# Performance work log

Measured on AMD Instinct MI355X. Metric: run time of the kernel, lower is better.

Reference implementation:

```python
import jax, jax.numpy as jnp
import numpy as np

D_IN = 4096
D_OUT = 4096
RANK = 16
NUM_EXPERTS = 8
TOP_K = 2
SCALING = 32.0 / RANK  # lora_alpha / r = 2.0


def setup_inputs() -> dict:
    key = jax.random.key(0)
    ks = jax.random.split(key, 6)
    x = jax.random.normal(ks[0], (4, 2048, D_IN), dtype=jnp.float32)
    W_base = jax.random.normal(ks[1], (D_OUT, D_IN), dtype=jnp.float32) * (1.0 / np.sqrt(D_IN))
    b_base = jax.random.normal(ks[2], (D_OUT,), dtype=jnp.float32) * 0.01
    W_router = jax.random.normal(ks[3], (NUM_EXPERTS, D_IN), dtype=jnp.float32) * 0.01
    # kaiming-uniform-like A; B nonzero (module inits B to zero, but zero B makes outputs/grads trivial)
    A_stack = jax.random.uniform(ks[4], (NUM_EXPERTS, RANK, D_IN), dtype=jnp.float32,
                                 minval=-1.0, maxval=1.0) * (1.0 / np.sqrt(D_IN))
    B_stack = jax.random.normal(ks[5], (NUM_EXPERTS, D_OUT, RANK), dtype=jnp.float32) * 0.02
    return {"x": x, "W_base": W_base, "b_base": b_base,
            "W_router": W_router, "A_stack": A_stack, "B_stack": B_stack}


def reference(x, W_base, b_base, W_router, A_stack, B_stack):
    orig_shape = x.shape
    xf = x.reshape(-1, D_IN)                                # [N, d_in]
    # Router: softmax -> top-k -> renormalize
    logits = xf @ W_router.T                                # [N, E]
    probs = jax.nn.softmax(logits, axis=-1)
    topk_p, topk_i = jax.lax.top_k(probs, TOP_K)            # [N, K]
    topk_p = topk_p / jnp.sum(topk_p, axis=-1, keepdims=True)
    # Combine weights per expert (scatter top-k probs into [N, E])
    combine = jnp.sum(jax.nn.one_hot(topk_i, NUM_EXPERTS, dtype=xf.dtype)
                      * topk_p[..., None], axis=1)          # [N, E]
    # Low-rank expert path: x @ A_e^T, weight, then @ B_e^T, summed over experts
    h = jnp.einsum('nd,erd->ner', xf, A_stack)              # [N, E, r]
    h = h * combine[..., None]
    lora_out = jnp.einsum('ner,eor->no', h, B_stack) * SCALING  # [N, d_out]
    base_out = xf @ W_base.T + b_base                       # [N, d_out]
    out = base_out + lora_out
    return out.reshape(orig_shape[:-1] + (D_OUT,))
```

## Files before the change

### kernel.cpp

```cpp
#include <hip/hip_runtime.h>

#define D_IN   4096
#define D_OUT  4096
#define N_TOK  8192
#define RANK   16
#define NEXP   8
#define ER     128
#define KCAT   4224
#define SCALING 2.0f

typedef __attribute__((ext_vector_type(8))) short short8;
typedef __attribute__((ext_vector_type(4))) float f32x4;
typedef __attribute__((ext_vector_type(4))) unsigned short us4;
typedef unsigned int uint;

__device__ __forceinline__ unsigned short f2bf(float f) {
  unsigned u = __float_as_uint(f);
  u += 0x7FFFu + ((u >> 16) & 1u);
  return (unsigned short)(u >> 16);
}

__device__ __forceinline__ void gload_lds16(const void* g, void* l) {
  __builtin_amdgcn_global_load_lds(
      (const __attribute__((address_space(1))) unsigned int*)g,
      (__attribute__((address_space(3))) unsigned int*)l, 16, 0, 0);
}

__global__ __launch_bounds__(256) void fused_prep_router_kernel(
    const float* __restrict__ X, const float* __restrict__ Wr,
    const float* __restrict__ W, const float* __restrict__ A,
    const float* __restrict__ B,
    unsigned short* __restrict__ Xcat, float* __restrict__ Comb,
    unsigned short* __restrict__ Wcat, unsigned short* __restrict__ Ab) {
  if (blockIdx.x < 512) {
    int wave = threadIdx.x >> 6, lane = threadIdx.x & 63;
    int tok0 = blockIdx.x * 16 + wave * 4;
    float acc[4][8];
#pragma unroll
    for (int t = 0; t < 4; ++t)
#pragma unroll
      for (int e = 0; e < 8; ++e) acc[t][e] = 0.f;
    const float4* X4 = (const float4*)X;
    const float4* W4 = (const float4*)Wr;
#pragma unroll 1
    for (int it = 0; it < 16; ++it) {
      int kq = it * 64 + lane;
      float4 w[8];
#pragma unroll
      for (int e = 0; e < 8; ++e) w[e] = W4[e * 1024 + kq];
#pragma unroll
      for (int t = 0; t < 4; ++t) {
        float4 xv = X4[(size_t)(tok0 + t) * 1024 + kq];
        us4 xb = { f2bf(xv.x), f2bf(xv.y), f2bf(xv.z), f2bf(xv.w) };
        ((us4*)(Xcat + (size_t)(tok0 + t) * KCAT))[kq] = xb;
#pragma unroll
        for (int e = 0; e < 8; ++e)
          acc[t][e] = fmaf(xv.x, w[e].x, fmaf(xv.y, w[e].y,
                       fmaf(xv.z, w[e].z, fmaf(xv.w, w[e].w, acc[t][e]))));
      }
    }
#pragma unroll
    for (int t = 0; t < 4; ++t)
#pragma unroll
      for (int e = 0; e < 8; ++e) {
        float v = acc[t][e];
        for (int off = 32; off; off >>= 1) v += __shfl_xor(v, off, 64);
        acc[t][e] = v;
      }
#pragma unroll
    for (int t = 0; t < 4; ++t) {
      float m1 = acc[t][0]; int i1 = 0;
#pragma unroll
      for (int e = 1; e < 8; ++e) if (acc[t][e] > m1) { m1 = acc[t][e]; i1 = e; }
      float m2 = -1e30f; int i2 = 0;
#pragma unroll
      for (int e = 0; e < 8; ++e)
        if (e != i1 && acc[t][e] > m2) { m2 = acc[t][e]; i2 = e; }
      float w1 = 1.f / (1.f + expf(m2 - m1));
      if (lane < 8) {
        float v = (lane == i1) ? w1 : (lane == i2) ? (1.f - w1) : 0.f;
        Comb[(size_t)(tok0 + t) * 8 + lane] = v * SCALING;
      }
    }
  } else {
    const int NW4 = (D_OUT * D_IN) / 4;
    const int NA4 = (ER * D_IN) / 4;
    const int NB4 = (D_OUT * ER) / 4;
    const int total = NW4 + NA4 + NB4;
    const int stride = 2048 * 256;
    for (int i = (blockIdx.x - 512) * blockDim.x + threadIdx.x; i < total;
         i += stride) {
      if (i < NW4) {
        float4 v = ((const float4*)W)[i];
        us4 o = { f2bf(v.x), f2bf(v.y), f2bf(v.z), f2bf(v.w) };
        int row = i >> 10, kq = i & 1023;
        ((us4*)(Wcat + (size_t)row * KCAT))[kq] = o;
      } else if (i < NW4 + NA4) {
        int j = i - NW4;
        float4 v = ((const float4*)A)[j];
        us4 o = { f2bf(v.x), f2bf(v.y), f2bf(v.z), f2bf(v.w) };
        ((us4*)Ab)[j] = o;
      } else {
        int j = i - NW4 - NA4;
        int o = j >> 5; int rem = j & 31; int e = rem >> 2; int rq = rem & 3;
        float4 v = *(const float4*)(B + (size_t)e * D_OUT * RANK + o * RANK + rq * 4);
        us4 ob = { f2bf(v.x), f2bf(v.y), f2bf(v.z), f2bf(v.w) };
        *(us4*)(Wcat + (size_t)o * KCAT + D_IN + e * 16 + rq * 4) = ob;
      }
    }
  }
}

#define HSTG(S) { const uint hbase = (S) * 40960u; \
  _Pragma("unroll") for (int c = 0; c < 2; ++c) { gload_lds16(pa[c], ldsc + hbase + da[c]); pa[c] += 128; } \
  _Pragma("unroll") for (int c = 0; c < 8; ++c) { gload_lds16(pb[c], ldsc + hbase + db[c]); pb[c] += 128; } }

#define HTILE(S, S2, DOSTG, VM) { const uint hb = (S) * 40960u; \
  short8 af[4]; short8 bfr[4][4]; \
  _Pragma("unroll") for (int kk = 0; kk < 4; ++kk) af[kk] = *(const short8*)(ldsc + hb + oA[kk]); \
  _Pragma("unroll") for (int n = 0; n < 4; ++n) \
    _Pragma("unroll") for (int kk = 0; kk < 4; ++kk) bfr[n][kk] = *(const short8*)(ldsc + hb + oB[n][kk]); \
  if (DOSTG) HSTG(S2); \
  __builtin_amdgcn_sched_barrier(0); __builtin_amdgcn_s_barrier(); __builtin_amdgcn_sched_barrier(0); \
  __builtin_amdgcn_s_setprio(1); \
  _Pragma("unroll") for (int kk = 0; kk < 4; ++kk) \
    _Pragma("unroll") for (int n = 0; n < 4; ++n) \
      acc[n] = __builtin_amdgcn_mfma_f32_16x16x32_bf16(af[kk], bfr[n][kk], acc[n], 0, 0, 0); \
  __builtin_amdgcn_s_setprio(0); \
  __builtin_amdgcn_sched_barrier(0); \
  asm volatile("s_waitcnt vmcnt(" #VM ")" ::: ); \
  __builtin_amdgcn_s_barrier(); __builtin_amdgcn_sched_barrier(0); }

__global__ __launch_bounds__(256, 1) void h_gemm_kernel(
    unsigned short* Xcat, const unsigned short* __restrict__ Ab,
    const float* __restrict__ Comb) {
  __shared__ unsigned short hlds[61440];
  char* ldsc = (char*)hlds;
  const int tid = threadIdx.x, wave = tid >> 6, lane = tid & 63;
  const int wm = wave >> 1, wn = wave & 1;
  const int row0 = blockIdx.x * 32;

  const unsigned short* pa[2]; uint da[2];
#pragma unroll
  for (int c = 0; c < 2; ++c) {
    int ch = c * 256 + tid, row = ch >> 4, s = ch & 15;
    pa[c] = Xcat + (size_t)(row0 + row) * KCAT + (s ^ ((row >> 1) & 7)) * 8;
    da[c] = (uint)ch * 16;
  }
  const unsigned short* pb[8]; uint db[8];
#pragma unroll
  for (int c = 0; c < 8; ++c) {
    int ch = c * 256 + tid, row = ch >> 4, s = ch & 15;
    pb[c] = Ab + (size_t)row * D_IN + (s ^ ((row >> 1) & 7)) * 8;
    db[c] = 8192u + (uint)ch * 16;
  }

  uint oA[4], oB[4][4];
  {
    int rA = wm * 16 + (lane & 15);
#pragma unroll
    for (int kk = 0; kk < 4; ++kk) {
      int slot = kk * 4 + (lane >> 4);
      oA[kk] = (uint)rA * 256 + (uint)((slot ^ ((rA >> 1) & 7)) * 16);
    }
#pragma unroll
    for (int n = 0; n < 4; ++n) {
      int rB = wn * 64 + n * 16 + (lane & 15);
#pragma unroll
      for (int kk = 0; kk < 4; ++kk) {
        int slot = kk * 4 + (lane >> 4);
        oB[n][kk] = 8192u + (uint)rB * 256 + (uint)((slot ^ ((rB >> 1) & 7)) * 16);
      }
    }
  }

  f32x4 acc[4];
#pragma unroll
  for (int n = 0; n < 4; ++n) acc[n] = (f32x4){0.f, 0.f, 0.f, 0.f};

  HSTG(0); HSTG(1);
  asm volatile("s_waitcnt vmcnt(10)" ::: );
  __builtin_amdgcn_s_barrier();
  __builtin_amdgcn_sched_barrier(0);

#pragma unroll 1
  for (int i3 = 0; i3 < 10; ++i3) {
    HTILE(0, 2, 1, 10);
    HTILE(1, 0, 1, 10);
    HTILE(2, 1, 1, 10);
  }
  HTILE(0, 0, 0, 0);
  HTILE(1, 0, 0, 0);

#pragma unroll
  for (int n = 0; n < 4; ++n) {
    int c = wn * 64 + n * 16 + (lane & 15);
    int e = c >> 4;
#pragma unroll
    for (int i = 0; i < 4; ++i) {
      int r = row0 + wm * 16 + (lane >> 4) * 4 + i;
      float v = acc[n][i] * Comb[(size_t)r * 8 + e];
      Xcat[(size_t)r * KCAT + D_IN + c] = f2bf(v);
    }
  }
}

#define STG_A(S) { gload_lds16(pA0, ldsc + (S) * 32768u + dA0); pA0 += 32; \
                   gload_lds16(pA1, ldsc + (S) * 32768u + dA1); pA1 += 32; }
#define STG_B(S) { gload_lds16(pB0, ldsc + (S) * 32768u + dB0); pB0 += 32; \
                   gload_lds16(pB1, ldsc + (S) * 32768u + dB1); pB1 += 32; }

#define MTILE(SLOT, SLOT3, DOSTG, VM) { \
  const uint sb = (SLOT) * 32768u; \
  short8 a0[4], bf[4], a1[4]; \
  _Pragma("unroll") for (int m = 0; m < 4; ++m) a0[m] = *(const short8*)(ldsc + sb + offA[m]); \
  _Pragma("unroll") for (int n = 0; n < 4; ++n) bf[n] = *(const short8*)(ldsc + sb + offB[n]); \
  _Pragma("unroll") for (int m = 0; m < 4; ++m) a1[m] = *(const short8*)(ldsc + sb + offA[4 + m]); \
  if (DOSTG) STG_A(SLOT3); \
  __builtin_amdgcn_sched_barrier(0); \
  __builtin_amdgcn_s_barrier(); \
  __builtin_amdgcn_sched_barrier(0); \
  __builtin_amdgcn_s_setprio(1); \
  _Pragma("unroll") for (int m = 0; m < 4; ++m) \
    _Pragma("unroll") for (int n = 0; n < 4; ++n) \
      acc[m][n] = __builtin_amdgcn_mfma_f32_16x16x32_bf16(a0[m], bf[n], acc[m][n], 0, 0, 0); \
  __builtin_amdgcn_s_setprio(0); \
  __builtin_amdgcn_sched_barrier(0); \
  __builtin_amdgcn_s_barrier(); \
  __builtin_amdgcn_sched_barrier(0); \
  if (DOSTG) STG_B(SLOT3); \
  __builtin_amdgcn_sched_barrier(0); \
  __builtin_amdgcn_s_barrier(); \
  __builtin_amdgcn_sched_barrier(0); \
  __builtin_amdgcn_s_setprio(1); \
  _Pragma("unroll") for (int m = 0; m < 4; ++m) \
    _Pragma("unroll") for (int n = 0; n < 4; ++n) \
      acc[4 + m][n] = __builtin_amdgcn_mfma_f32_16x16x32_bf16(a1[m], bf[n], acc[4 + m][n], 0, 0, 0); \
  __builtin_amdgcn_s_setprio(0); \
  __builtin_amdgcn_sched_barrier(0); \
  asm volatile("s_waitcnt vmcnt(" #VM ")" ::: ); \
  __builtin_amdgcn_s_barrier(); \
  __builtin_amdgcn_sched_barrier(0); }

__global__ __launch_bounds__(512, 2) void main_gemm_kernel(
    const unsigned short* __restrict__ Xcat, const unsigned short* __restrict__ Wcat,
    const float* __restrict__ bias, float* __restrict__ Out) {
  __shared__ unsigned short lds[4 * 16384];
  char* ldsc = (char*)lds;
  const int tid = threadIdx.x;
  const int wave = tid >> 6, lane = tid & 63;
  const int wm = wave >> 2, wn = wave & 3;
  const int ks = lane >> 4;

  int bid = blockIdx.x;
  int swz = (bid & 7) * 64 + (bid >> 3);
  int mb = swz >> 4, nb = swz & 15;
  const int row0 = mb * 256, col0 = nb * 256;

  const unsigned short *pA0, *pA1, *pB0, *pB1;
  uint dA0, dA1, dB0, dB1;
  {
    int ch0 = tid, ch1 = 512 + tid;
    int rr0 = ch0 >> 2, ss0 = (ch0 & 3) ^ ((ch0 >> 3) & 3);
    int rr1 = ch1 >> 2, ss1 = (ch1 & 3) ^ ((ch1 >> 3) & 3);
    pA0 = Xcat + (size_t)(row0 + rr0) * KCAT + ss0 * 8;
    pA1 = Xcat + (size_t)(row0 + rr1) * KCAT + ss1 * 8;
    pB0 = Wcat + (size_t)(col0 + rr0) * KCAT + ss0 * 8;
    pB1 = Wcat + (size_t)(col0 + rr1) * KCAT + ss1 * 8;
    dA0 = (uint)wave * 1024;          dA1 = 8192u + (uint)wave * 1024;
    dB0 = 16384u + (uint)wave * 1024; dB1 = 24576u + (uint)wave * 1024;
  }

  uint offA[8], offB[4];
#pragma unroll
  for (int mi = 0; mi < 8; ++mi) {
    int r = wm * 128 + mi * 16 + (lane & 15);
    offA[mi] = (uint)r * 64 + (uint)((ks ^ ((r >> 1) & 3)) * 16);
  }
#pragma unroll
  for (int ni = 0; ni < 4; ++ni) {
    int r = wn * 64 + ni * 16 + (lane & 15);
    offB[ni] = 16384u + (uint)r * 64 + (uint)((ks ^ ((r >> 1) & 3)) * 16);
  }

  f32x4 acc[8][4];
#pragma unroll
  for (int mi = 0; mi < 8; ++mi)
#pragma unroll
    for (int ni = 0; ni < 4; ++ni) acc[mi][ni] = (f32x4){0.f, 0.f, 0.f, 0.f};

  STG_A(0); STG_B(0); STG_A(1); STG_B(1); STG_A(2); STG_B(2);
  asm volatile("s_waitcnt vmcnt(8)" ::: );
  __builtin_amdgcn_s_barrier();
  __builtin_amdgcn_sched_barrier(0);

#pragma unroll 1
  for (int i4 = 0; i4 < 32; ++i4) {
    MTILE(0, 3, 1, 8);
    MTILE(1, 0, 1, 8);
    MTILE(2, 1, 1, 8);
    MTILE(3, 2, 1, 8);
  }
  MTILE(0, 3, 1, 8);
  MTILE(1, 0, 0, 4);
  MTILE(2, 0, 0, 0);
  MTILE(3, 0, 0, 0);

#pragma unroll
  for (int ni = 0; ni < 4; ++ni) {
    const int c = col0 + wn * 64 + ni * 16 + (lane & 15);
    const float bv = bias[c];
#pragma unroll
    for (int mi = 0; mi < 8; ++mi) {
#pragma unroll
      for (int i = 0; i < 4; ++i) {
        int r = row0 + wm * 128 + mi * 16 + ks * 4 + i;
        Out[(size_t)r * D_OUT + c] = acc[mi][ni][i] + bv;
      }
    }
  }
}

extern "C" void kernel_launch(void* const* d_in, const int* in_sizes, int n_in,
                              void* d_out, int out_size, void* d_ws, size_t ws_size,
                              hipStream_t stream) {
  const float* x        = (const float*)d_in[0];
  const float* W_base   = (const float*)d_in[1];
  const float* b_base   = (const float*)d_in[2];
  const float* W_router = (const float*)d_in[3];
  const float* A_stack  = (const float*)d_in[4];
  const float* B_stack  = (const float*)d_in[5];
  float* out = (float*)d_out;

  char* ws = (char*)d_ws;
  unsigned short* Xcat = (unsigned short*)(ws);
  unsigned short* Wcat = (unsigned short*)(ws + 69206016);
  unsigned short* Ab   = (unsigned short*)(ws + 103809024);
  float*          Comb = (float*)(ws + 104857600);

  hipLaunchKernelGGL(fused_prep_router_kernel, dim3(2560), dim3(256), 0, stream,
                     x, W_router, W_base, A_stack, B_stack, Xcat, Comb, Wcat, Ab);
  hipLaunchKernelGGL(h_gemm_kernel, dim3(256), dim3(256), 0, stream,
                     Xcat, Ab, Comb);
  hipLaunchKernelGGL(main_gemm_kernel, dim3(512), dim3(512), 0, stream,
                     Xcat, Wcat, b_base, out);
}
```

Before: 341.3 us.

## Prefetch next k-tile LDS fragments into ping-pong registers during MFMA phases

Result: no change. 340.4 us (-0.3%).

```diff
diff --git a/kernel.cpp b/kernel.cpp
--- a/kernel.cpp
+++ b/kernel.cpp
@@ -210,35 +210,46 @@
 #define STG_B(S) { gload_lds16(pB0, ldsc + (S) * 32768u + dB0); pB0 += 32; \
                    gload_lds16(pB1, ldsc + (S) * 32768u + dB1); pB1 += 32; }
 
-#define MTILE(SLOT, SLOT3, DOSTG, VM) { \
+#define MT(SLOT, SLOT3, DOSTG, VMTOK, aCur, bCur, aNxt, bNxt, RDNEXT, LGTOK) { \
   const uint sb = (SLOT) * 32768u; \
-  short8 a0[4], bf[4], a1[4]; \
-  _Pragma("unroll") for (int m = 0; m < 4; ++m) a0[m] = *(const short8*)(ldsc + sb + offA[m]); \
-  _Pragma("unroll") for (int n = 0; n < 4; ++n) bf[n] = *(const short8*)(ldsc + sb + offB[n]); \
-  _Pragma("unroll") for (int m = 0; m < 4; ++m) a1[m] = *(const short8*)(ldsc + sb + offA[4 + m]); \
+  const uint sbn = (((SLOT) + 1) & 3) * 32768u; \
+   \
+  _Pragma("unroll") for (int m = 0; m < 4; ++m) \
+    a1r[m] = *(const short8*)(ldsc + sb + offA[4 + m]); \
   if (DOSTG) STG_A(SLOT3); \
   __builtin_amdgcn_sched_barrier(0); \
   __builtin_amdgcn_s_barrier(); \
+  __builtin_amdgcn_sched_barrier(0); \
+  asm volatile("s_waitcnt lgkmcnt(4)" ::: ); \
   __builtin_amdgcn_sched_barrier(0); \
   __builtin_amdgcn_s_setprio(1); \
   _Pragma("unroll") for (int m = 0; m < 4; ++m) \
     _Pragma("unroll") for (int n = 0; n < 4; ++n) \
-      acc[m][n] = __builtin_amdgcn_mfma_f32_16x16x32_bf16(a0[m], bf[n], acc[m][n], 0, 0, 0); \
+      acc[m][n] = __builtin_amdgcn_mfma_f32_16x16x32_bf16(aCur[m], bCur[n], acc[m][n], 0, 0, 0); \
   __builtin_amdgcn_s_setprio(0); \
   __builtin_amdgcn_sched_barrier(0); \
+  asm volatile("s_waitcnt " VMTOK ::: ); \
   __builtin_amdgcn_s_barrier(); \
   __builtin_amdgcn_sched_barrier(0); \
+   \
+  if (RDNEXT) { \
+    _Pragma("unroll") for (int m = 0; m < 4; ++m) \
+      aNxt[m] = *(const short8*)(ldsc + sbn + offA[m]); \
+    _Pragma("unroll") for (int n = 0; n < 4; ++n) \
+      bNxt[n] = *(const short8*)(ldsc + sbn + offB[n]); \
+  } \
   if (DOSTG) STG_B(SLOT3); \
   __builtin_amdgcn_sched_barrier(0); \
   __builtin_amdgcn_s_barrier(); \
+  __builtin_amdgcn_sched_barrier(0); \
+  asm volatile("s_waitcnt " LGTOK ::: ); \
   __builtin_amdgcn_sched_barrier(0); \
   __builtin_amdgcn_s_setprio(1); \
   _Pragma("unroll") for (int m = 0; m < 4; ++m) \
     _Pragma("unroll") for (int n = 0; n < 4; ++n) \
-      acc[4 + m][n] = __builtin_amdgcn_mfma_f32_16x16x32_bf16(a1[m], bf[n], acc[4 + m][n], 0, 0, 0); \
+      acc[4 + m][n] = __builtin_amdgcn_mfma_f32_16x16x32_bf16(a1r[m], bCur[n], acc[4 + m][n], 0, 0, 0); \
   __builtin_amdgcn_s_setprio(0); \
   __builtin_amdgcn_sched_barrier(0); \
-  asm volatile("s_waitcnt vmcnt(" #VM ")" ::: ); \
   __builtin_amdgcn_s_barrier(); \
   __builtin_amdgcn_sched_barrier(0); }
 
@@ -289,22 +300,29 @@
 #pragma unroll
     for (int ni = 0; ni < 4; ++ni) acc[mi][ni] = (f32x4){0.f, 0.f, 0.f, 0.f};
 
+  short8 aAr[4], bAr[4], aBr[4], bBr[4], a1r[4];
+
   STG_A(0); STG_B(0); STG_A(1); STG_B(1); STG_A(2); STG_B(2);
   asm volatile("s_waitcnt vmcnt(8)" ::: );
   __builtin_amdgcn_s_barrier();
   __builtin_amdgcn_sched_barrier(0);
+#pragma unroll
+  for (int m = 0; m < 4; ++m) aAr[m] = *(const short8*)(ldsc + offA[m]);
+#pragma unroll
+  for (int n = 0; n < 4; ++n) bAr[n] = *(const short8*)(ldsc + offB[n]);
+  __builtin_amdgcn_sched_barrier(0);
 
 #pragma unroll 1
   for (int i4 = 0; i4 < 32; ++i4) {
-    MTILE(0, 3, 1, 8);
-    MTILE(1, 0, 1, 8);
-    MTILE(2, 1, 1, 8);
-    MTILE(3, 2, 1, 8);
-  }
-  MTILE(0, 3, 1, 8);
-  MTILE(1, 0, 0, 4);
-  MTILE(2, 0, 0, 0);
-  MTILE(3, 0, 0, 0);
+    MT(0, 3, 1, "vmcnt(6)", aAr, bAr, aBr, bBr, 1, "lgkmcnt(8)");
+    MT(1, 0, 1, "vmcnt(6)", aBr, bBr, aAr, bAr, 1, "lgkmcnt(8)");
+    MT(2, 1, 1, "vmcnt(6)", aAr, bAr, aBr, bBr, 1, "lgkmcnt(8)");
+    MT(3, 2, 1, "vmcnt(6)", aBr, bBr, aAr, bAr, 1, "lgkmcnt(8)");
+  }
+  MT(0, 3, 1, "vmcnt(6)", aAr, bAr, aBr, bBr, 1, "lgkmcnt(8)");
+  MT(1, 0, 0, "vmcnt(4)", aBr, bBr, aAr, bAr, 1, "lgkmcnt(8)");
+  MT(2, 0, 0, "vmcnt(0)", aAr, bAr, aBr, bBr, 1, "lgkmcnt(8)");
+  MT(3, 0, 0, "vmcnt(0)", aBr, bBr, aAr, bAr, 0, "lgkmcnt(0)");
 
 #pragma unroll
   for (int ni = 0; ni < 4; ++ni) {
```

## Shrink main GEMM tile to 128x128 with 4 waves and 3-stage pipeline

Applied to the files above, without the earlier changes.

Measured after the change: 468.9 us. 1.37x slower.

```diff
diff --git a/kernel.cpp b/kernel.cpp
--- a/kernel.cpp
+++ b/kernel.cpp
@@ -205,116 +205,102 @@
   }
 }
 
-#define STG_A(S) { gload_lds16(pA0, ldsc + (S) * 32768u + dA0); pA0 += 32; \
-                   gload_lds16(pA1, ldsc + (S) * 32768u + dA1); pA1 += 32; }
-#define STG_B(S) { gload_lds16(pB0, ldsc + (S) * 32768u + dB0); pB0 += 32; \
-                   gload_lds16(pB1, ldsc + (S) * 32768u + dB1); pB1 += 32; }
-
-#define MTILE(SLOT, SLOT3, DOSTG, VM) { \
-  const uint sb = (SLOT) * 32768u; \
-  short8 a0[4], bf[4], a1[4]; \
-  _Pragma("unroll") for (int m = 0; m < 4; ++m) a0[m] = *(const short8*)(ldsc + sb + offA[m]); \
-  _Pragma("unroll") for (int n = 0; n < 4; ++n) bf[n] = *(const short8*)(ldsc + sb + offB[n]); \
-  _Pragma("unroll") for (int m = 0; m < 4; ++m) a1[m] = *(const short8*)(ldsc + sb + offA[4 + m]); \
-  if (DOSTG) STG_A(SLOT3); \
+#define STG(S) { \
+  gload_lds16(pA0, ldsc + (S) * 16384u + dA0); pA0 += 32; \
+  gload_lds16(pA1, ldsc + (S) * 16384u + dA1); pA1 += 32; \
+  gload_lds16(pB0, ldsc + (S) * 16384u + dB0); pB0 += 32; \
+  gload_lds16(pB1, ldsc + (S) * 16384u + dB1); pB1 += 32; }
+
+#define MT(SLOT, SLOTN, DOSTG, VM) { \
+  const uint sb = (SLOT) * 16384u; \
+  short8 a[4], b[4]; \
+  _Pragma("unroll") for (int m = 0; m < 4; ++m) a[m] = *(const short8*)(ldsc + sb + offA[m]); \
+  _Pragma("unroll") for (int n = 0; n < 4; ++n) b[n] = *(const short8*)(ldsc + sb + offB[n]); \
+  if (DOSTG) STG(SLOTN); \
   __builtin_amdgcn_sched_barrier(0); \
   __builtin_amdgcn_s_barrier(); \
   __builtin_amdgcn_sched_barrier(0); \
   __builtin_amdgcn_s_setprio(1); \
   _Pragma("unroll") for (int m = 0; m < 4; ++m) \
     _Pragma("unroll") for (int n = 0; n < 4; ++n) \
-      acc[m][n] = __builtin_amdgcn_mfma_f32_16x16x32_bf16(a0[m], bf[n], acc[m][n], 0, 0, 0); \
-  __builtin_amdgcn_s_setprio(0); \
-  __builtin_amdgcn_sched_barrier(0); \
-  __builtin_amdgcn_s_barrier(); \
-  __builtin_amdgcn_sched_barrier(0); \
-  if (DOSTG) STG_B(SLOT3); \
-  __builtin_amdgcn_sched_barrier(0); \
-  __builtin_amdgcn_s_barrier(); \
-  __builtin_amdgcn_sched_barrier(0); \
-  __builtin_amdgcn_s_setprio(1); \
-  _Pragma("unroll") for (int m = 0; m < 4; ++m) \
-    _Pragma("unroll") for (int n = 0; n < 4; ++n) \
-      acc[4 + m][n] = __builtin_amdgcn_mfma_f32_16x16x32_bf16(a1[m], bf[n], acc[4 + m][n], 0, 0, 0); \
+      acc[m][n] = __builtin_amdgcn_mfma_f32_16x16x32_bf16(a[m], b[n], acc[m][n], 0, 0, 0); \
   __builtin_amdgcn_s_setprio(0); \
   __builtin_amdgcn_sched_barrier(0); \
   asm volatile("s_waitcnt vmcnt(" #VM ")" ::: ); \
   __builtin_amdgcn_s_barrier(); \
   __builtin_amdgcn_sched_barrier(0); }
 
-__global__ __launch_bounds__(512, 2) void main_gemm_kernel(
+__global__ __launch_bounds__(256, 3) void main_gemm_kernel(
     const unsigned short* __restrict__ Xcat, const unsigned short* __restrict__ Wcat,
     const float* __restrict__ bias, float* __restrict__ Out) {
-  __shared__ unsigned short lds[4 * 16384];
+  __shared__ unsigned short lds[3 * 8192];
   char* ldsc = (char*)lds;
   const int tid = threadIdx.x;
   const int wave = tid >> 6, lane = tid & 63;
-  const int wm = wave >> 2, wn = wave & 3;
+  const int wm = wave >> 1, wn = wave & 1;
   const int ks = lane >> 4;
 
   int bid = blockIdx.x;
-  int swz = (bid & 7) * 64 + (bid >> 3);
-  int mb = swz >> 4, nb = swz & 15;
-  const int row0 = mb * 256, col0 = nb * 256;
+  int swz = (bid & 7) * 256 + (bid >> 3);
+  int mb = swz >> 5, nb = swz & 31;
+  const int row0 = mb * 128, col0 = nb * 128;
 
   const unsigned short *pA0, *pA1, *pB0, *pB1;
   uint dA0, dA1, dB0, dB1;
   {
-    int ch0 = tid, ch1 = 512 + tid;
+    int ch0 = tid, ch1 = 256 + tid;
     int rr0 = ch0 >> 2, ss0 = (ch0 & 3) ^ ((ch0 >> 3) & 3);
     int rr1 = ch1 >> 2, ss1 = (ch1 & 3) ^ ((ch1 >> 3) & 3);
     pA0 = Xcat + (size_t)(row0 + rr0) * KCAT + ss0 * 8;
     pA1 = Xcat + (size_t)(row0 + rr1) * KCAT + ss1 * 8;
     pB0 = Wcat + (size_t)(col0 + rr0) * KCAT + ss0 * 8;
     pB1 = Wcat + (size_t)(col0 + rr1) * KCAT + ss1 * 8;
-    dA0 = (uint)wave * 1024;          dA1 = 8192u + (uint)wave * 1024;
-    dB0 = 16384u + (uint)wave * 1024; dB1 = 24576u + (uint)wave * 1024;
-  }
-
-  uint offA[8], offB[4];
-#pragma unroll
-  for (int mi = 0; mi < 8; ++mi) {
-    int r = wm * 128 + mi * 16 + (lane & 15);
+    dA0 = (uint)ch0 * 16;          dA1 = (uint)ch1 * 16;
+    dB0 = 8192u + (uint)ch0 * 16;  dB1 = 8192u + (uint)ch1 * 16;
+  }
+
+  uint offA[4], offB[4];
+#pragma unroll
+  for (int mi = 0; mi < 4; ++mi) {
+    int r = wm * 64 + mi * 16 + (lane & 15);
     offA[mi] = (uint)r * 64 + (uint)((ks ^ ((r >> 1) & 3)) * 16);
   }
 #pragma unroll
   for (int ni = 0; ni < 4; ++ni) {
     int r = wn * 64 + ni * 16 + (lane & 15);
-    offB[ni] = 16384u + (uint)r * 64 + (uint)((ks ^ ((r >> 1) & 3)) * 16);
-  }
-
-  f32x4 acc[8][4];
-#pragma unroll
-  for (int mi = 0; mi < 8; ++mi)
+    offB[ni] = 8192u + (uint)r * 64 + (uint)((ks ^ ((r >> 1) & 3)) * 16);
+  }
+
+  f32x4 acc[4][4];
+#pragma unroll
+  for (int mi = 0; mi < 4; ++mi)
 #pragma unroll
     for (int ni = 0; ni < 4; ++ni) acc[mi][ni] = (f32x4){0.f, 0.f, 0.f, 0.f};
 
-  STG_A(0); STG_B(0); STG_A(1); STG_B(1); STG_A(2); STG_B(2);
-  asm volatile("s_waitcnt vmcnt(8)" ::: );
+  STG(0); STG(1);
+  asm volatile("s_waitcnt vmcnt(4)" ::: );
   __builtin_amdgcn_s_barrier();
   __builtin_amdgcn_sched_barrier(0);
 
 #pragma unroll 1
-  for (int i4 = 0; i4 < 32; ++i4) {
-    MTILE(0, 3, 1, 8);
-    MTILE(1, 0, 1, 8);
-    MTILE(2, 1, 1, 8);
-    MTILE(3, 2, 1, 8);
-  }
-  MTILE(0, 3, 1, 8);
-  MTILE(1, 0, 0, 4);
-  MTILE(2, 0, 0, 0);
-  MTILE(3, 0, 0, 0);
+  for (int i3 = 0; i3 < 43; ++i3) {
+    MT(0, 2, 1, 4);
+    MT(1, 0, 1, 4);
+    MT(2, 1, 1, 4);
+  }
+  MT(0, 2, 1, 4);
+  MT(1, 0, 0, 0);
+  MT(2, 0, 0, 0);
 
 #pragma unroll
   for (int ni = 0; ni < 4; ++ni) {
     const int c = col0 + wn * 64 + ni * 16 + (lane & 15);
     const float bv = bias[c];
 #pragma unroll
-    for (int mi = 0; mi < 8; ++mi) {
+    for (int mi = 0; mi < 4; ++mi) {
 #pragma unroll
       for (int i = 0; i < 4; ++i) {
-        int r = row0 + wm * 128 + mi * 16 + ks * 4 + i;
+        int r = row0 + wm * 64 + mi * 16 + ks * 4 + i;
         Out[(size_t)r * D_OUT + c] = acc[mi][ni][i] + bv;
       }
     }
@@ -342,6 +328,6 @@
                      x, W_router, W_base, A_stack, B_stack, Xcat, Comb, Wcat, Ab);
   hipLaunchKernelGGL(h_gemm_kernel, dim3(256), dim3(256), 0, stream,
                      Xcat, Ab, Comb);
-  hipLaunchKernelGGL(main_gemm_kernel, dim3(512), dim3(512), 0, stream,
+  hipLaunchKernelGGL(main_gemm_kernel, dim3(2048), dim3(256), 0, stream,
                      Xcat, Wcat, b_base, out);
 }
```

## Overlap weight bf16 conversion with LoRA h-GEMM and defer a1 LDS loads

Applied to the files above, without the earlier changes.

Result: slower. 362.8 us (+6.3%).

```diff
diff --git a/kernel.cpp b/kernel.cpp
--- a/kernel.cpp
+++ b/kernel.cpp
@@ -26,87 +26,64 @@
       (__attribute__((address_space(3))) unsigned int*)l, 16, 0, 0);
 }
 
-__global__ __launch_bounds__(256) void fused_prep_router_kernel(
+__global__ __launch_bounds__(256) void router_kernel(
     const float* __restrict__ X, const float* __restrict__ Wr,
-    const float* __restrict__ W, const float* __restrict__ A,
-    const float* __restrict__ B,
+    const float* __restrict__ A,
     unsigned short* __restrict__ Xcat, float* __restrict__ Comb,
-    unsigned short* __restrict__ Wcat, unsigned short* __restrict__ Ab) {
-  if (blockIdx.x < 512) {
-    int wave = threadIdx.x >> 6, lane = threadIdx.x & 63;
-    int tok0 = blockIdx.x * 16 + wave * 4;
-    float acc[4][8];
-#pragma unroll
-    for (int t = 0; t < 4; ++t)
-#pragma unroll
-      for (int e = 0; e < 8; ++e) acc[t][e] = 0.f;
-    const float4* X4 = (const float4*)X;
-    const float4* W4 = (const float4*)Wr;
+    unsigned short* __restrict__ Ab) {
+  {
+    int j = blockIdx.x * 256 + threadIdx.x;
+    float4 v = ((const float4*)A)[j];
+    us4 o = { f2bf(v.x), f2bf(v.y), f2bf(v.z), f2bf(v.w) };
+    ((us4*)Ab)[j] = o;
+  }
+  int wave = threadIdx.x >> 6, lane = threadIdx.x & 63;
+  int tok0 = blockIdx.x * 16 + wave * 4;
+  float acc[4][8];
+#pragma unroll
+  for (int t = 0; t < 4; ++t)
+#pragma unroll
+    for (int e = 0; e < 8; ++e) acc[t][e] = 0.f;
+  const float4* X4 = (const float4*)X;
+  const float4* W4 = (const float4*)Wr;
 #pragma unroll 1
-    for (int it = 0; it < 16; ++it) {
-      int kq = it * 64 + lane;
-      float4 w[8];
-#pragma unroll
-      for (int e = 0; e < 8; ++e) w[e] = W4[e * 1024 + kq];
-#pragma unroll
-      for (int t = 0; t < 4; ++t) {
-        float4 xv = X4[(size_t)(tok0 + t) * 1024 + kq];
-        us4 xb = { f2bf(xv.x), f2bf(xv.y), f2bf(xv.z), f2bf(xv.w) };
-        ((us4*)(Xcat + (size_t)(tok0 + t) * KCAT))[kq] = xb;
-#pragma unroll
-        for (int e = 0; e < 8; ++e)
-          acc[t][e] = fmaf(xv.x, w[e].x, fmaf(xv.y, w[e].y,
-                       fmaf(xv.z, w[e].z, fmaf(xv.w, w[e].w, acc[t][e]))));
-      }
-    }
-#pragma unroll
-    for (int t = 0; t < 4; ++t)
-#pragma unroll
-      for (int e = 0; e < 8; ++e) {
-        float v = acc[t][e];
-        for (int off = 32; off; off >>= 1) v += __shfl_xor(v, off, 64);
-        acc[t][e] = v;
-      }
+  for (int it = 0; it < 16; ++it) {
+    int kq = it * 64 + lane;
+    float4 w[8];
+#pragma unroll
+    for (int e = 0; e < 8; ++e) w[e] = W4[e * 1024 + kq];
 #pragma unroll
     for (int t = 0; t < 4; ++t) {
-      float m1 = acc[t][0]; int i1 = 0;
-#pragma unroll
-      for (int e = 1; e < 8; ++e) if (acc[t][e] > m1) { m1 = acc[t][e]; i1 = e; }
-      float m2 = -1e30f; int i2 = 0;
+      float4 xv = X4[(size_t)(tok0 + t) * 1024 + kq];
+      us4 xb = { f2bf(xv.x), f2bf(xv.y), f2bf(xv.z), f2bf(xv.w) };
+      ((us4*)(Xcat + (size_t)(tok0 + t) * KCAT))[kq] = xb;
 #pragma unroll
       for (int e = 0; e < 8; ++e)
-        if (e != i1 && acc[t][e] > m2) { m2 = acc[t][e]; i2 = e; }
-      float w1 = 1.f / (1.f + expf(m2 - m1));
-      if (lane < 8) {
-        float v = (lane == i1) ? w1 : (lane == i2) ? (1.f - w1) : 0.f;
-        Comb[(size_t)(tok0 + t) * 8 + lane] = v * SCALING;
-      }
-    }
-  } else {
-    const int NW4 = (D_OUT * D_IN) / 4;
-    const int NA4 = (ER * D_IN) / 4;
-    const int NB4 = (D_OUT * ER) / 4;
-    const int total = NW4 + NA4 + NB4;
-    const int stride = 2048 * 256;
-    for (int i = (blockIdx.x - 512) * blockDim.x + threadIdx.x; i < total;
-         i += stride) {
-      if (i < NW4) {
-        float4 v = ((const float4*)W)[i];
-        us4 o = { f2bf(v.x), f2bf(v.y), f2bf(v.z), f2bf(v.w) };
-        int row = i >> 10, kq = i & 1023;
-        ((us4*)(Wcat + (size_t)row * KCAT))[kq] = o;
-      } else if (i < NW4 + NA4) {
-        int j = i - NW4;
-        float4 v = ((const float4*)A)[j];
-        us4 o = { f2bf(v.x), f2bf(v.y), f2bf(v.z), f2bf(v.w) };
-        ((us4*)Ab)[j] = o;
-      } else {
-        int j = i - NW4 - NA4;
-        int o = j >> 5; int rem = j & 31; int e = rem >> 2; int rq = rem & 3;
-        float4 v = *(const float4*)(B + (size_t)e * D_OUT * RANK + o * RANK + rq * 4);
-        us4 ob = { f2bf(v.x), f2bf(v.y), f2bf(v.z), f2bf(v.w) };
-        *(us4*)(Wcat + (size_t)o * KCAT + D_IN + e * 16 + rq * 4) = ob;
-      }
+        acc[t][e] = fmaf(xv.x, w[e].x, fmaf(xv.y, w[e].y,
+                     fmaf(xv.z, w[e].z, fmaf(xv.w, w[e].w, acc[t][e]))));
+    }
+  }
+#pragma unroll
+  for (int t = 0; t < 4; ++t)
+#pragma unroll
+    for (int e = 0; e < 8; ++e) {
+      float v = acc[t][e];
+      for (int off = 32; off; off >>= 1) v += __shfl_xor(v, off, 64);
+      acc[t][e] = v;
+    }
+#pragma unroll
+  for (int t = 0; t < 4; ++t) {
+    float m1 = acc[t][0]; int i1 = 0;
+#pragma unroll
+    for (int e = 1; e < 8; ++e) if (acc[t][e] > m1) { m1 = acc[t][e]; i1 = e; }
+    float m2 = -1e30f; int i2 = 0;
+#pragma unroll
+    for (int e = 0; e < 8; ++e)
+      if (e != i1 && acc[t][e] > m2) { m2 = acc[t][e]; i2 = e; }
+    float w1 = 1.f / (1.f + expf(m2 - m1));
+    if (lane < 8) {
+      float v = (lane == i1) ? w1 : (lane == i2) ? (1.f - w1) : 0.f;
+      Comb[(size_t)(tok0 + t) * 8 + lane] = v * SCALING;
     }
   }
 }
@@ -131,10 +108,34 @@
   asm volatile("s_waitcnt vmcnt(" #VM ")" ::: ); \
   __builtin_amdgcn_s_barrier(); __builtin_amdgcn_sched_barrier(0); }
 
-__global__ __launch_bounds__(256, 1) void h_gemm_kernel(
+__global__ __launch_bounds__(256, 1) void h_prep_kernel(
     unsigned short* Xcat, const unsigned short* __restrict__ Ab,
-    const float* __restrict__ Comb) {
+    const float* __restrict__ Comb,
+    const float* __restrict__ W, const float* __restrict__ B,
+    unsigned short* __restrict__ Wcat) {
   __shared__ unsigned short hlds[61440];
+  if (blockIdx.x >= 256) {
+    const int NW4 = (D_OUT * D_IN) / 4;
+    const int NB4 = (D_OUT * ER) / 4;
+    const int total = NW4 + NB4;
+    const int stride = 2048 * 256;
+    for (int i = (blockIdx.x - 256) * blockDim.x + threadIdx.x; i < total;
+         i += stride) {
+      if (i < NW4) {
+        float4 v = ((const float4*)W)[i];
+        us4 o = { f2bf(v.x), f2bf(v.y), f2bf(v.z), f2bf(v.w) };
+        int row = i >> 10, kq = i & 1023;
+        ((us4*)(Wcat + (size_t)row * KCAT))[kq] = o;
+      } else {
+        int j = i - NW4;
+        int o = j >> 5; int rem = j & 31; int e = rem >> 2; int rq = rem & 3;
+        float4 v = *(const float4*)(B + (size_t)e * D_OUT * RANK + o * RANK + rq * 4);
+        us4 ob = { f2bf(v.x), f2bf(v.y), f2bf(v.z), f2bf(v.w) };
+        *(us4*)(Wcat + (size_t)o * KCAT + D_IN + e * 16 + rq * 4) = ob;
+      }
+    }
+    return;
+  }
   char* ldsc = (char*)hlds;
   const int tid = threadIdx.x, wave = tid >> 6, lane = tid & 63;
   const int wm = wave >> 1, wn = wave & 1;
@@ -215,7 +216,6 @@
   short8 a0[4], bf[4], a1[4]; \
   _Pragma("unroll") for (int m = 0; m < 4; ++m) a0[m] = *(const short8*)(ldsc + sb + offA[m]); \
   _Pragma("unroll") for (int n = 0; n < 4; ++n) bf[n] = *(const short8*)(ldsc + sb + offB[n]); \
-  _Pragma("unroll") for (int m = 0; m < 4; ++m) a1[m] = *(const short8*)(ldsc + sb + offA[4 + m]); \
   if (DOSTG) STG_A(SLOT3); \
   __builtin_amdgcn_sched_barrier(0); \
   __builtin_amdgcn_s_barrier(); \
@@ -228,6 +228,7 @@
   __builtin_amdgcn_sched_barrier(0); \
   __builtin_amdgcn_s_barrier(); \
   __builtin_amdgcn_sched_barrier(0); \
+  _Pragma("unroll") for (int m = 0; m < 4; ++m) a1[m] = *(const short8*)(ldsc + sb + offA[4 + m]); \
   if (DOSTG) STG_B(SLOT3); \
   __builtin_amdgcn_sched_barrier(0); \
   __builtin_amdgcn_s_barrier(); \
@@ -338,10 +339,10 @@
   unsigned short* Ab   = (unsigned short*)(ws + 103809024);
   float*          Comb = (float*)(ws + 104857600);
 
-  hipLaunchKernelGGL(fused_prep_router_kernel, dim3(2560), dim3(256), 0, stream,
-                     x, W_router, W_base, A_stack, B_stack, Xcat, Comb, Wcat, Ab);
-  hipLaunchKernelGGL(h_gemm_kernel, dim3(256), dim3(256), 0, stream,
-                     Xcat, Ab, Comb);
+  hipLaunchKernelGGL(router_kernel, dim3(512), dim3(256), 0, stream,
+                     x, W_router, A_stack, Xcat, Comb, Ab);
+  hipLaunchKernelGGL(h_prep_kernel, dim3(2304), dim3(256), 0, stream,
+                     Xcat, Ab, Comb, W_base, B_stack, Wcat);
   hipLaunchKernelGGL(main_gemm_kernel, dim3(512), dim3(512), 0, stream,
                      Xcat, Wcat, b_base, out);
 }
```
